# Kernel optimization log

Measured on AMD Instinct MI355X. Metric: run time of the kernel, lower is better.

## Reference

```python
import jax, jax.numpy as jnp
import numpy as np

N = 50000      # num nodes
E = 1_200_000  # num edges
NID = 92       # node_input_dim
ED = 1         # edge_input_dim
H = 64         # hidden_dim
L = 5          # num_layers
EMB = 64       # embedding_dim
G = 256        # num graphs in batch
EPS = 1e-5


def _glorot(key, shape):
    fan_in, fan_out = shape[-2], shape[-1]
    lim = float(np.sqrt(6.0 / (fan_in + fan_out)))
    return jax.random.uniform(key, shape, jnp.float32, -lim, lim)


def setup_inputs() -> dict:
    key = jax.random.key(0)
    ks = jax.random.split(key, 16)
    inp = {
        "x": jax.random.normal(ks[0], (N, NID), jnp.float32),
        "edge_attr": jax.random.uniform(ks[1], (E, ED), jnp.float32),
        "edge_index": jax.random.randint(ks[2], (2, E), 0, N, jnp.int32),
        "batch": jnp.sort(jax.random.randint(ks[3], (N,), 0, G, jnp.int32)),
        # node embedding
        "node_W": _glorot(ks[4], (NID, H)),
        "node_b": jnp.zeros((H,), jnp.float32),
        # per-layer message net: Linear(2H+ED,H) -> BN -> SiLU -> Linear(H,H)
        "msg_W1": _glorot(ks[5], (L, 2 * H + ED, H)),
        "msg_b1": jnp.zeros((L, H), jnp.float32),
        "msg_g1": jnp.ones((L, H), jnp.float32),
        "msg_be1": jnp.zeros((L, H), jnp.float32),
        "msg_W2": _glorot(ks[6], (L, H, H)),
        "msg_b2": jnp.zeros((L, H), jnp.float32),
        # per-layer update net: Linear(2H,H) -> BN -> SiLU
        "upd_W": _glorot(ks[7], (L, 2 * H, H)),
        "upd_b": jnp.zeros((L, H), jnp.float32),
        "upd_g": jnp.ones((L, H), jnp.float32),
        "upd_be": jnp.zeros((L, H), jnp.float32),
        # output projection
        "out_W": _glorot(ks[8], (H, EMB)),
        "out_b": jnp.zeros((EMB,), jnp.float32),
    }
    return inp


def _bn(z, g, b):
    # BatchNorm1d, training-mode batch statistics (biased variance), eps=1e-5
    mu = jnp.mean(z, axis=0)
    var = jnp.var(z, axis=0)
    return (z - mu) * jax.lax.rsqrt(var + EPS) * g + b


def reference(x, edge_attr, node_W, node_b, msg_W1, msg_b1, msg_g1, msg_be1,
              msg_W2, msg_b2, upd_W, upd_b, upd_g, upd_be, out_W, out_b,
              edge_index, batch):
    src, dst = edge_index[0], edge_index[1]  # PyG: x_j = x[src], x_i = x[dst]
    h = x @ node_W + node_b                  # [N, H]
    deg = jax.ops.segment_sum(jnp.ones((E,), h.dtype), dst, num_segments=N)
    deg = jnp.maximum(deg, 1.0)[:, None]     # mean aggregation denominator
    for l in range(L):
        # message: cat([x_i, x_j, edge_attr]) -> Linear -> BN -> SiLU -> Linear
        m = jnp.concatenate([h[dst], h[src], edge_attr], axis=1)  # [E, 2H+ED]
        m = _bn(m @ msg_W1[l] + msg_b1[l], msg_g1[l], msg_be1[l])
        m = jax.nn.silu(m) @ msg_W2[l] + msg_b2[l]                # [E, H]
        # aggregate: scatter-mean to destination nodes
        agg = jax.ops.segment_sum(m, dst, num_segments=N) / deg   # [N, H]
        # update: cat([x, agg]) -> Linear -> BN -> SiLU
        u = jnp.concatenate([h, agg], axis=1) @ upd_W[l] + upd_b[l]
        h = jax.nn.silu(_bn(u, upd_g[l], upd_be[l]))              # [N, H]
    # global mean pool over graphs
    cnt = jnp.maximum(jax.ops.segment_sum(jnp.ones((N,), h.dtype), batch, num_segments=G), 1.0)
    g = jax.ops.segment_sum(h, batch, num_segments=G) / cnt[:, None]  # [G, H]
    return jax.nn.silu(g @ out_W + out_b)                              # [G, EMB]
```

## Files before the change

kernel.cpp:

```cpp
#include <hip/hip_runtime.h>
#include <hip/hip_bf16.h>

#define NN 50000
#define EE 1200000
#define GG 256
#define LL 5

__device__ __forceinline__ float silu_f(float x) {
    return x * __builtin_amdgcn_rcpf(1.0f + __expf(-x));
}
__device__ __forceinline__ int rfl(int x) { return __builtin_amdgcn_readfirstlane(x); }

__global__ __launch_bounds__(256) void k_hist(const int* __restrict__ ei, int* __restrict__ fill, int E) {
    int e = blockIdx.x * 256 + threadIdx.x;
    if (e < E) atomicAdd(&fill[ei[E + e]], 1);
}

__global__ __launch_bounds__(256) void k_scan_blk(int* __restrict__ fill, int* __restrict__ rowptr,
                                                  float* __restrict__ degf, int* __restrict__ bsum, int n) {
    __shared__ int wsum[4];
    int tid = threadIdx.x, lane = tid & 63, wid = tid >> 6;
    int i = blockIdx.x * 256 + tid;
    int v = (i < n) ? fill[i] : 0;
    int x = v;
    #pragma unroll
    for (int off = 1; off < 64; off <<= 1) {
        int t = __shfl_up(x, off);
        if (lane >= off) x += t;
    }
    if (lane == 63) wsum[wid] = x;
    __syncthreads();
    int waveoff = 0;
    if (wid > 0) waveoff += wsum[0];
    if (wid > 1) waveoff += wsum[1];
    if (wid > 2) waveoff += wsum[2];
    int inc = x + waveoff;
    if (i < n) {
        rowptr[i + 1] = inc;
        degf[i] = (float)(v > 0 ? v : 1);
        fill[i] = 0;
    }
    if (tid == 255) bsum[blockIdx.x] = inc;
}

__global__ __launch_bounds__(256) void k_scan_top(int* __restrict__ bsum, int B) {
    __shared__ int wsum[4];
    int tid = threadIdx.x, lane = tid & 63, wid = tid >> 6;
    int v = (tid < B) ? bsum[tid] : 0;
    int x = v;
    #pragma unroll
    for (int off = 1; off < 64; off <<= 1) {
        int t = __shfl_up(x, off);
        if (lane >= off) x += t;
    }
    if (lane == 63) wsum[wid] = x;
    __syncthreads();
    int waveoff = 0;
    if (wid > 0) waveoff += wsum[0];
    if (wid > 1) waveoff += wsum[1];
    if (wid > 2) waveoff += wsum[2];
    if (tid < B) bsum[tid] = x + waveoff;
}

__global__ __launch_bounds__(256) void k_scan_add(const int* __restrict__ bsum, int* __restrict__ rowptr, int n) {
    int b = blockIdx.x;
    int i = b * 256 + threadIdx.x;
    if (i < n) {
        int add = (b > 0) ? bsum[b - 1] : 0;
        rowptr[i + 1] += add;
    }
    if (i == 0) rowptr[0] = 0;
}

__global__ __launch_bounds__(256) void k_scatter(const int* __restrict__ ei, const float* __restrict__ ea,
                                                 const int* __restrict__ rowptr, int* __restrict__ fill,
                                                 unsigned int* __restrict__ edata, int E) {
    int e = blockIdx.x * 256 + threadIdx.x;
    if (e < E) {
        int d = ei[E + e];
        int pos = atomicAdd(&fill[d], 1);
        int idx = rowptr[d] + pos;
        int ea15 = (int)(ea[e] * 32768.0f + 0.5f);
        if (ea15 > 32767) ea15 = 32767;
        edata[idx] = ((unsigned int)ea15 << 17) | (unsigned int)ei[e];
    }
}

__global__ __launch_bounds__(256) void k_fold(const float* __restrict__ msg_W2, const float* __restrict__ msg_b2,
                                              const float* __restrict__ upd_W, float* __restrict__ W2p,
                                              float* __restrict__ b2p) {
    int l = blockIdx.x;
    const float* W2 = msg_W2 + (size_t)l * 4096;
    const float* U2 = upd_W + (size_t)l * 8192 + 4096;
    int lane = threadIdx.x & 63, wid = threadIdx.x >> 6;
    for (int ii = 0; ii < 16; ii++) {
        int i = rfl(wid * 16 + ii);
        float acc = 0.0f;
        for (int k = 0; k < 64; k++) acc = fmaf(W2[i * 64 + k], U2[k * 64 + lane], acc);
        W2p[(size_t)l * 4096 + i * 64 + lane] = acc;
    }
    if (wid == 0) {
        float acc = 0.0f;
        for (int k = 0; k < 64; k++) acc = fmaf(msg_b2[l * 64 + k], U2[k * 64 + lane], acc);
        b2p[l * 64 + lane] = acc;
    }
}

__global__ __launch_bounds__(256) void k_node_emb(const float* __restrict__ x, const float* __restrict__ W,
                                                  const float* __restrict__ b, float* __restrict__ h, int n) {
    __shared__ float sW[92 * 64];
    for (int i = threadIdx.x; i < 92 * 64; i += 256) sW[i] = W[i];
    __syncthreads();
    int lane = threadIdx.x & 63;
    int gw = (blockIdx.x * 256 + threadIdx.x) >> 6;
    int nw = (gridDim.x * 256) >> 6;
    float bj = b[lane];
    int tiles = n >> 3;
    for (int t = gw; t < tiles; t += nw) {
        int rb = rfl(t << 3);
        float acc[8];
        #pragma unroll
        for (int r = 0; r < 8; r++) acc[r] = bj;
        for (int kb = 0; kb < 80; kb += 16) {
            float wv[16];
            #pragma unroll
            for (int t2 = 0; t2 < 16; t2++) wv[t2] = sW[(kb + t2) * 64 + lane];
            #pragma unroll
            for (int r = 0; r < 8; r++) {
                const float* xr = x + (size_t)(rb + r) * 92 + kb;
                #pragma unroll
                for (int t2 = 0; t2 < 16; t2++) acc[r] = fmaf(xr[t2], wv[t2], acc[r]);
            }
        }
        {
            float wv[12];
            #pragma unroll
            for (int t2 = 0; t2 < 12; t2++) wv[t2] = sW[(80 + t2) * 64 + lane];
            #pragma unroll
            for (int r = 0; r < 8; r++) {
                const float* xr = x + (size_t)(rb + r) * 92 + 80;
                #pragma unroll
                for (int t2 = 0; t2 < 12; t2++) acc[r] = fmaf(xr[t2], wv[t2], acc[r]);
            }
        }
        #pragma unroll
        for (int r = 0; r < 8; r++) h[(size_t)(rb + r) * 64 + lane] = acc[r];
    }
}

__global__ __launch_bounds__(256) void k_node_pre(const float* __restrict__ h, const float* __restrict__ W1,
                                                  const float* __restrict__ b1, float* __restrict__ Hd,
                                                  _Float16* __restrict__ Hs, int n) {
    __shared__ float sA[4096], sB[4096];
    for (int i = threadIdx.x; i < 4096; i += 256) { sA[i] = W1[i]; sB[i] = W1[4096 + i]; }
    __syncthreads();
    int lane = threadIdx.x & 63;
    int gw = (blockIdx.x * 256 + threadIdx.x) >> 6;
    int nw = (gridDim.x * 256) >> 6;
    float bj = b1[lane];
    int tiles = n >> 3;
    for (int t = gw; t < tiles; t += nw) {
        int rb = rfl(t << 3);
        float accA[8], accB[8];
        #pragma unroll
        for (int r = 0; r < 8; r++) { accA[r] = bj; accB[r] = 0.0f; }
        for (int kb = 0; kb < 64; kb += 16) {
            float wA[16], wB[16];
            #pragma unroll
            for (int t2 = 0; t2 < 16; t2++) { wA[t2] = sA[(kb + t2) * 64 + lane]; wB[t2] = sB[(kb + t2) * 64 + lane]; }
            #pragma unroll
            for (int r = 0; r < 8; r++) {
                const float* hr = h + (size_t)(rb + r) * 64 + kb;
                #pragma unroll
                for (int t2 = 0; t2 < 16; t2++) {
                    float hk = hr[t2];
                    accA[r] = fmaf(hk, wA[t2], accA[r]);
                    accB[r] = fmaf(hk, wB[t2], accB[r]);
                }
            }
        }
        #pragma unroll
        for (int r = 0; r < 8; r++) {
            Hd[(size_t)(rb + r) * 64 + lane] = accA[r];
            Hs[(size_t)(rb + r) * 64 + lane] = (_Float16)accB[r];
        }
    }
}

__global__ __launch_bounds__(256) void k_bn_pre(const float* __restrict__ u, const float* __restrict__ usum,
                                                const float* __restrict__ usq, const float* __restrict__ g,
                                                const float* __restrict__ be, const float* __restrict__ W1,
                                                const float* __restrict__ b1, float* __restrict__ h,
                                                float* __restrict__ Hd, _Float16* __restrict__ Hs,
                                                int n, float invN) {
    __shared__ float sA[4096], sB[4096];
    __shared__ float sH[4][8][64];
    for (int i = threadIdx.x; i < 4096; i += 256) { sA[i] = W1[i]; sB[i] = W1[4096 + i]; }
    __syncthreads();
    int lane = threadIdx.x & 63, wid = threadIdx.x >> 6;
    float mean = usum[lane] * invN;
    float var = usq[lane] * invN - mean * mean;
    float inv = rsqrtf(var + 1e-5f);
    float sc = inv * g[lane];
    float sh = fmaf(-mean, sc, be[lane]);
    float bj = b1[lane];
    int gw = (blockIdx.x * 256 + threadIdx.x) >> 6;
    int nw = (gridDim.x * 256) >> 6;
    int tiles = n >> 3;
    for (int t = gw; t < tiles; t += nw) {
        int rb = rfl(t << 3);
        #pragma unroll
        for (int r = 0; r < 8; r++) {
            float uv = u[(size_t)(rb + r) * 64 + lane];
            float hv = silu_f(fmaf(uv, sc, sh));
            h[(size_t)(rb + r) * 64 + lane] = hv;
            sH[wid][r][lane] = hv;
        }
        float accA[8], accB[8];
        #pragma unroll
        for (int r = 0; r < 8; r++) { accA[r] = bj; accB[r] = 0.0f; }
        for (int k = 0; k < 64; k += 2) {
            float wA0 = sA[k * 64 + lane],       wB0 = sB[k * 64 + lane];
            float wA1 = sA[(k + 1) * 64 + lane], wB1 = sB[(k + 1) * 64 + lane];
            #pragma unroll
            for (int r = 0; r < 8; r++) {
                float h0 = sH[wid][r][k], h1 = sH[wid][r][k + 1];
                accA[r] = fmaf(h0, wA0, accA[r]);
                accB[r] = fmaf(h0, wB0, accB[r]);
                accA[r] = fmaf(h1, wA1, accA[r]);
                accB[r] = fmaf(h1, wB1, accB[r]);
            }
        }
        #pragma unroll
        for (int r = 0; r < 8; r++) {
            Hd[(size_t)(rb + r) * 64 + lane] = accA[r];
            Hs[(size_t)(rb + r) * 64 + lane] = (_Float16)accB[r];
        }
    }
}

__global__ __launch_bounds__(256) void k_edge_stats(const float* __restrict__ Hd, const _Float16* __restrict__ Hs,
                                                    const int* __restrict__ rowptr, const unsigned int* __restrict__ edata,
                                                    const float* __restrict__ w1e,
                                                    float* __restrict__ esum, float* __restrict__ esq, int n) {
    __shared__ float rs[4][64], rq[4][64];
    int wid = threadIdx.x >> 6, lane = threadIdx.x & 63;
    int gw = (blockIdx.x * 256 + threadIdx.x) >> 6;
    int nw = (gridDim.x * 256) >> 6;
    float wj = w1e[lane] * (1.0f / 32768.0f);
    float s = 0.0f, q = 0.0f;
    for (int node = gw; node < n; node += nw) {
        int nu = rfl(node);
        int e0 = rowptr[nu], e1 = rowptr[nu + 1];
        if (e0 == e1) continue;
        float hd = Hd[(size_t)nu * 64 + lane];
        int e = e0;
        for (; e + 16 <= e1; e += 16) {
            float hs[16], av[16];
            #pragma unroll
            for (int j = 0; j < 16; j++) {
                unsigned int p = edata[e + j];
                int sidx = rfl((int)(p & 0x1FFFFu));
                av[j] = (float)rfl((int)(p >> 17));
                hs[j] = (float)Hs[(size_t)sidx * 64 + lane];
            }
            #pragma unroll
            for (int j = 0; j < 16; j++) {
                float z = fmaf(av[j], wj, hd) + hs[j];
                s += z;
                q = fmaf(z, z, q);
            }
        }
        for (; e + 8 <= e1; e += 8) {
            float hs[8], av[8];
            #pragma unroll
            for (int j = 0; j < 8; j++) {
                unsigned int p = edata[e + j];
                int sidx = rfl((int)(p & 0x1FFFFu));
                av[j] = (float)rfl((int)(p >> 17));
                hs[j] = (float)Hs[(size_t)sidx * 64 + lane];
            }
            #pragma unroll
            for (int j = 0; j < 8; j++) {
                float z = fmaf(av[j], wj, hd) + hs[j];
                s += z;
                q = fmaf(z, z, q);
            }
        }
        for (; e < e1; e++) {
            unsigned int p = edata[e];
            int sidx = rfl((int)(p & 0x1FFFFu));
            float a = (float)rfl((int)(p >> 17));
            float z = fmaf(a, wj, hd) + (float)Hs[(size_t)sidx * 64 + lane];
            s += z;
            q = fmaf(z, z, q);
        }
    }
    rs[wid][lane] = s; rq[wid][lane] = q;
    __syncthreads();
    if (wid == 0) {
        float ts = rs[0][lane] + rs[1][lane] + rs[2][lane] + rs[3][lane];
        float tq = rq[0][lane] + rq[1][lane] + rq[2][lane] + rq[3][lane];
        atomicAdd(&esum[lane], ts);
        atomicAdd(&esq[lane], tq);
    }
}

__global__ __launch_bounds__(256) void k_agg_upd(const float* __restrict__ Hd, const _Float16* __restrict__ Hs,
                                                 const int* __restrict__ rowptr, const unsigned int* __restrict__ edata,
                                                 const float* __restrict__ w1e,
                                                 const float* __restrict__ esum, const float* __restrict__ esq,
                                                 const float* __restrict__ g1, const float* __restrict__ be1,
                                                 const float* __restrict__ degf,
                                                 const float* __restrict__ h, const float* __restrict__ U1,
                                                 const float* __restrict__ W2p, const float* __restrict__ b2p,
                                                 const float* __restrict__ ub,
                                                 float* __restrict__ u, float* __restrict__ usum,
                                                 float* __restrict__ usq, int n, float invE) {
    __shared__ float sU[4096], sP[4096];
    __shared__ float2 sHA[4][4][64];
    for (int i = threadIdx.x; i < 4096; i += 256) { sU[i] = U1[i]; sP[i] = W2p[i]; }
    __syncthreads();
    int lane = threadIdx.x & 63, wid = threadIdx.x >> 6;
    float mean = esum[lane] * invE;
    float var = esq[lane] * invE - mean * mean;
    float inv = rsqrtf(var + 1e-5f);
    float sc = inv * g1[lane];
    float sh = fmaf(-mean, sc, be1[lane]);
    float wj = w1e[lane] * (1.0f / 32768.0f);
    float b2j = b2p[lane], ubj = ub[lane];
    int gw = (blockIdx.x * 256 + threadIdx.x) >> 6;
    int nw = (gridDim.x * 256) >> 6;
    float s = 0.0f, q = 0.0f;
    int tiles = n >> 2;
    for (int t = gw; t < tiles; t += nw) {
        int rb = rfl(t << 2);
        float gate[4];
        for (int r = 0; r < 4; r++) {
            int nu = rb + r;
            int e0 = rowptr[nu], e1 = rowptr[nu + 1];
            gate[r] = (e1 > e0) ? 1.0f : 0.0f;
            float hd = Hd[(size_t)nu * 64 + lane];
            float acc = 0.0f;
            int e = e0;
            for (; e + 16 <= e1; e += 16) {
                float hs[16], av[16];
                #pragma unroll
                for (int j = 0; j < 16; j++) {
                    unsigned int p = edata[e + j];
                    int sidx = rfl((int)(p & 0x1FFFFu));
                    av[j] = (float)rfl((int)(p >> 17));
                    hs[j] = (float)Hs[(size_t)sidx * 64 + lane];
                }
                #pragma unroll
                for (int j = 0; j < 16; j++) {
                    float z = fmaf(av[j], wj, hd) + hs[j];
                    acc += silu_f(fmaf(z, sc, sh));
                }
            }
            for (; e + 8 <= e1; e += 8) {
                float hs[8], av[8];
                #pragma unroll
                for (int j = 0; j < 8; j++) {
                    unsigned int p = edata[e + j];
                    int sidx = rfl((int)(p & 0x1FFFFu));
                    av[j] = (float)rfl((int)(p >> 17));
                    hs[j] = (float)Hs[(size_t)sidx * 64 + lane];
                }
                #pragma unroll
                for (int j = 0; j < 8; j++) {
                    float z = fmaf(av[j], wj, hd) + hs[j];
                    acc += silu_f(fmaf(z, sc, sh));
                }
            }
            for (; e < e1; e++) {
                unsigned int p = edata[e];
                int sidx = rfl((int)(p & 0x1FFFFu));
                float a = (float)rfl((int)(p >> 17));
                float z = fmaf(a, wj, hd) + (float)Hs[(size_t)sidx * 64 + lane];
                acc += silu_f(fmaf(z, sc, sh));
            }
            float hv = h[(size_t)nu * 64 + lane];
            sHA[wid][r][lane] = make_float2(hv, acc / degf[nu]);
        }
        float accu[4];
        #pragma unroll
        for (int r = 0; r < 4; r++) accu[r] = fmaf(gate[r], b2j, ubj);
        for (int k = 0; k < 64; k++) {
            float wU = sU[k * 64 + lane], wP = sP[k * 64 + lane];
            #pragma unroll
            for (int r = 0; r < 4; r++) {
                float2 ha = sHA[wid][r][k];
                accu[r] = fmaf(ha.x, wU, accu[r]);
                accu[r] = fmaf(ha.y, wP, accu[r]);
            }
        }
        #pragma unroll
        for (int r = 0; r < 4; r++) {
            u[(size_t)(rb + r) * 64 + lane] = accu[r];
            s += accu[r];
            q = fmaf(accu[r], accu[r], q);
        }
    }
    {
        float* my = (float*)&sHA[wid][0][0];
        my[lane] = s;
        my[64 + lane] = q;
    }
    __syncthreads();
    if (wid == 0) {
        float ts = 0.0f, tq = 0.0f;
        #pragma unroll
        for (int w = 0; w < 4; w++) {
            const float* b = (const float*)&sHA[w][0][0];
            ts += b[lane];
            tq += b[64 + lane];
        }
        atomicAdd(&usum[lane], ts);
        atomicAdd(&usq[lane], tq);
    }
}

__global__ __launch_bounds__(256) void k_bn_pool(const float* __restrict__ u, const float* __restrict__ usum,
                                                 const float* __restrict__ usq, const float* __restrict__ g,
                                                 const float* __restrict__ be, const int* __restrict__ batch,
                                                 float* __restrict__ gsum, float* __restrict__ gcnt,
                                                 int n, float invN) {
    __shared__ float ssc[64], ssh[64];
    if (threadIdx.x < 64) {
        int j = threadIdx.x;
        float mean = usum[j] * invN;
        float var = usq[j] * invN - mean * mean;
        float inv = rsqrtf(var + 1e-5f);
        float sc = inv * g[j];
        ssc[j] = sc;
        ssh[j] = fmaf(-mean, sc, be[j]);
    }
    __syncthreads();
    int lane = threadIdx.x & 63;
    int gw = (blockIdx.x * 256 + threadIdx.x) >> 6;
    int nw = (gridDim.x * 256) >> 6;
    int per = (n + nw - 1) / nw;
    int start = gw * per;
    int end = start + per; if (end > n) end = n;
    if (start >= end) return;
    float sc = ssc[lane], sh = ssh[lane];
    int cur = batch[start];
    float acc = 0.0f, c = 0.0f;
    for (int i = start; i < end; i++) {
        int b = batch[i];
        if (b != cur) {
            atomicAdd(&gsum[(size_t)cur * 64 + lane], acc);
            if (lane == 0) atomicAdd(&gcnt[cur], c);
            cur = b; acc = 0.0f; c = 0.0f;
        }
        float y = fmaf(u[(size_t)i * 64 + lane], sc, sh);
        acc += silu_f(y);
        c += 1.0f;
    }
    atomicAdd(&gsum[(size_t)cur * 64 + lane], acc);
    if (lane == 0) atomicAdd(&gcnt[cur], c);
}

__global__ __launch_bounds__(256) void k_out(const float* __restrict__ gsum, const float* __restrict__ gcnt,
                                             const float* __restrict__ OW, const float* __restrict__ ob,
                                             float* __restrict__ out, int G) {
    __shared__ float sW[4096];
    for (int i = threadIdx.x; i < 4096; i += 256) sW[i] = OW[i];
    __syncthreads();
    int lane = threadIdx.x & 63;
    int gw = (blockIdx.x * 256 + threadIdx.x) >> 6;
    int nw = (gridDim.x * 256) >> 6;
    for (int g = gw; g < G; g += nw) {
        int gu = rfl(g);
        float c = gcnt[gu]; if (c < 1.0f) c = 1.0f;
        float ci = 1.0f / c;
        float acc = ob[lane];
        const float* gr = gsum + (size_t)gu * 64;
        #pragma unroll
        for (int k = 0; k < 64; k++) acc = fmaf(gr[k] * ci, sW[k * 64 + lane], acc);
        out[(size_t)gu * 64 + lane] = silu_f(acc);
    }
}

extern "C" void kernel_launch(void* const* d_in, const int* in_sizes, int n_in,
                              void* d_out, int out_size, void* d_ws, size_t ws_size,
                              hipStream_t stream) {
    const int N = NN, E = EE, G = GG, L = LL;
    const float* x         = (const float*)d_in[0];
    const float* edge_attr = (const float*)d_in[1];
    const int*   edge_index= (const int*)d_in[2];
    const int*   batch     = (const int*)d_in[3];
    const float* node_W    = (const float*)d_in[4];
    const float* node_b    = (const float*)d_in[5];
    const float* msg_W1    = (const float*)d_in[6];
    const float* msg_b1    = (const float*)d_in[7];
    const float* msg_g1    = (const float*)d_in[8];
    const float* msg_be1   = (const float*)d_in[9];
    const float* msg_W2    = (const float*)d_in[10];
    const float* msg_b2    = (const float*)d_in[11];
    const float* upd_W     = (const float*)d_in[12];
    const float* upd_b     = (const float*)d_in[13];
    const float* upd_g     = (const float*)d_in[14];
    const float* upd_be    = (const float*)d_in[15];
    const float* out_W     = (const float*)d_in[16];
    const float* out_b     = (const float*)d_in[17];
    float* out = (float*)d_out;

    char* ws = (char*)d_ws;
    size_t off = 0;
    auto alloc = [&](size_t b) { size_t o = off; off = (off + b + 255) & ~(size_t)255; return o; };
    float* h    = (float*)(ws + alloc((size_t)N * 64 * 4));
    float* Hd   = (float*)(ws + alloc((size_t)N * 64 * 4));
    _Float16* Hs = (_Float16*)(ws + alloc((size_t)N * 64 * 2));
    unsigned int* edata = (unsigned int*)(ws + alloc((size_t)E * 4));
    int* rowptr = (int*)  (ws + alloc((size_t)(N + 1) * 4));
    float* degf = (float*)(ws + alloc((size_t)N * 4));
    float* W2p  = (float*)(ws + alloc((size_t)L * 4096 * 4));
    float* b2p  = (float*)(ws + alloc((size_t)L * 64 * 4));
    int* bsum   = (int*)  (ws + alloc((size_t)256 * 4));
    size_t zero_begin = off;
    int*   fill = (int*)  (ws + alloc((size_t)N * 4));
    float* stats= (float*)(ws + alloc((size_t)L * 4 * 64 * 4));
    float* gsum = (float*)(ws + alloc((size_t)(G * 64 + G) * 4));
    size_t zero_end = off;
    float* gcnt = gsum + (size_t)G * 64;
    float* u = Hd;

    hipMemsetAsync(ws + zero_begin, 0, zero_end - zero_begin, stream);

    const int SB = (N + 255) / 256;
    k_hist<<<(E + 255) / 256, 256, 0, stream>>>(edge_index, fill, E);
    k_scan_blk<<<SB, 256, 0, stream>>>(fill, rowptr, degf, bsum, N);
    k_scan_top<<<1, 256, 0, stream>>>(bsum, SB);
    k_scan_add<<<SB, 256, 0, stream>>>(bsum, rowptr, N);
    k_scatter<<<(E + 255) / 256, 256, 0, stream>>>(edge_index, edge_attr, rowptr, fill, edata, E);

    k_fold<<<L, 256, 0, stream>>>(msg_W2, msg_b2, upd_W, W2p, b2p);
    k_node_emb<<<1024, 256, 0, stream>>>(x, node_W, node_b, h, N);

    k_node_pre<<<1024, 256, 0, stream>>>(h, msg_W1, msg_b1, Hd, Hs, N);

    for (int l = 0; l < L; l++) {
        const float* W1  = msg_W1 + (size_t)l * 129 * 64;
        const float* w1e = W1 + 128 * 64;
        float* esum = stats + (size_t)l * 256;
        float* esq  = esum + 64;
        float* usum = esum + 128;
        float* usq  = esum + 192;
        k_edge_stats<<<2048, 256, 0, stream>>>(Hd, Hs, rowptr, edata, w1e, esum, esq, N);
        k_agg_upd<<<1024, 256, 0, stream>>>(Hd, Hs, rowptr, edata, w1e, esum, esq,
                                            msg_g1 + l * 64, msg_be1 + l * 64, degf,
                                            h, upd_W + (size_t)l * 8192, W2p + (size_t)l * 4096,
                                            b2p + (size_t)l * 64, upd_b + l * 64,
                                            u, usum, usq, N, 1.0f / E);
        if (l < L - 1) {
            const float* W1n = msg_W1 + (size_t)(l + 1) * 129 * 64;
            k_bn_pre<<<1024, 256, 0, stream>>>(u, usum, usq, upd_g + l * 64, upd_be + l * 64,
                                               W1n, msg_b1 + (l + 1) * 64, h, Hd, Hs, N, 1.0f / N);
        } else {
            k_bn_pool<<<256, 256, 0, stream>>>(u, usum, usq, upd_g + l * 64, upd_be + l * 64,
                                               batch, gsum, gcnt, N, 1.0f / N);
        }
    }

    k_out<<<64, 256, 0, stream>>>(gsum, gcnt, out_W, out_b, out, G);
}
```

Baseline: 1.187 ms.

## Precompute update-net h·U1 term in node pre-pass and stage x rows in LDS

The h-part of the update linear (h @ U1 + ub) moves out of the edge aggregation kernel and into the node pre-pass kernels, which now compute three 64x64 products per node and write a new Hu buffer. The aggregation kernel then only multiplies the aggregated messages by the folded W2' matrix, which shrinks its LDS footprint and inner loop, and its grid grows. The node embedding kernel stages each wave's 8 input rows in shared memory with float4 loads instead of scalar global reads. The pre-pass kernels use 4-row tiles with more LDS and an extra N×64 float buffer that must be written and read, and h is still written in full.

```diff
diff --git a/kernel.cpp b/kernel.cpp
--- a/kernel.cpp
+++ b/kernel.cpp
@@ -109,15 +109,21 @@
 __global__ __launch_bounds__(256) void k_node_emb(const float* __restrict__ x, const float* __restrict__ W,
                                                   const float* __restrict__ b, float* __restrict__ h, int n) {
     __shared__ float sW[92 * 64];
+    __shared__ float sX[4][736];
     for (int i = threadIdx.x; i < 92 * 64; i += 256) sW[i] = W[i];
     __syncthreads();
-    int lane = threadIdx.x & 63;
+    int lane = threadIdx.x & 63, wid = threadIdx.x >> 6;
     int gw = (blockIdx.x * 256 + threadIdx.x) >> 6;
     int nw = (gridDim.x * 256) >> 6;
     float bj = b[lane];
     int tiles = n >> 3;
     for (int t = gw; t < tiles; t += nw) {
         int rb = rfl(t << 3);
+        const float4* xb = (const float4*)(x + (size_t)rb * 92);
+        float4* sx4 = (float4*)&sX[wid][0];
+        sx4[lane] = xb[lane];
+        sx4[lane + 64] = xb[lane + 64];
+        if (lane < 56) sx4[lane + 128] = xb[lane + 128];
         float acc[8];
         #pragma unroll
         for (int r = 0; r < 8; r++) acc[r] = bj;
@@ -127,9 +133,8 @@
             for (int t2 = 0; t2 < 16; t2++) wv[t2] = sW[(kb + t2) * 64 + lane];
             #pragma unroll
             for (int r = 0; r < 8; r++) {
-                const float* xr = x + (size_t)(rb + r) * 92 + kb;
-                #pragma unroll
-                for (int t2 = 0; t2 < 16; t2++) acc[r] = fmaf(xr[t2], wv[t2], acc[r]);
+                #pragma unroll
+                for (int t2 = 0; t2 < 16; t2++) acc[r] = fmaf(sX[wid][r * 92 + kb + t2], wv[t2], acc[r]);
             }
         }
         {
@@ -138,9 +143,8 @@
             for (int t2 = 0; t2 < 12; t2++) wv[t2] = sW[(80 + t2) * 64 + lane];
             #pragma unroll
             for (int r = 0; r < 8; r++) {
-                const float* xr = x + (size_t)(rb + r) * 92 + 80;
-                #pragma unroll
-                for (int t2 = 0; t2 < 12; t2++) acc[r] = fmaf(xr[t2], wv[t2], acc[r]);
+                #pragma unroll
+                for (int t2 = 0; t2 < 12; t2++) acc[r] = fmaf(sX[wid][r * 92 + 80 + t2], wv[t2], acc[r]);
             }
         }
         #pragma unroll
@@ -149,40 +153,48 @@
 }
 
 __global__ __launch_bounds__(256) void k_node_pre(const float* __restrict__ h, const float* __restrict__ W1,
-                                                  const float* __restrict__ b1, float* __restrict__ Hd,
-                                                  _Float16* __restrict__ Hs, int n) {
-    __shared__ float sA[4096], sB[4096];
-    for (int i = threadIdx.x; i < 4096; i += 256) { sA[i] = W1[i]; sB[i] = W1[4096 + i]; }
-    __syncthreads();
-    int lane = threadIdx.x & 63;
-    int gw = (blockIdx.x * 256 + threadIdx.x) >> 6;
-    int nw = (gridDim.x * 256) >> 6;
-    float bj = b1[lane];
-    int tiles = n >> 3;
+                                                  const float* __restrict__ b1, const float* __restrict__ U1,
+                                                  const float* __restrict__ ub, float* __restrict__ Hd,
+                                                  _Float16* __restrict__ Hs, float* __restrict__ Hu, int n) {
+    __shared__ float sA[4096], sB[4096], sU[4096];
+    __shared__ float sH[4][256];
+    for (int i = threadIdx.x; i < 4096; i += 256) { sA[i] = W1[i]; sB[i] = W1[4096 + i]; sU[i] = U1[i]; }
+    __syncthreads();
+    int lane = threadIdx.x & 63, wid = threadIdx.x >> 6;
+    int gw = (blockIdx.x * 256 + threadIdx.x) >> 6;
+    int nw = (gridDim.x * 256) >> 6;
+    float bj = b1[lane], uj = ub[lane];
+    int tiles = n >> 2;
     for (int t = gw; t < tiles; t += nw) {
-        int rb = rfl(t << 3);
-        float accA[8], accB[8];
-        #pragma unroll
-        for (int r = 0; r < 8; r++) { accA[r] = bj; accB[r] = 0.0f; }
-        for (int kb = 0; kb < 64; kb += 16) {
-            float wA[16], wB[16];
-            #pragma unroll
-            for (int t2 = 0; t2 < 16; t2++) { wA[t2] = sA[(kb + t2) * 64 + lane]; wB[t2] = sB[(kb + t2) * 64 + lane]; }
-            #pragma unroll
-            for (int r = 0; r < 8; r++) {
-                const float* hr = h + (size_t)(rb + r) * 64 + kb;
-                #pragma unroll
-                for (int t2 = 0; t2 < 16; t2++) {
-                    float hk = hr[t2];
+        int rb = rfl(t << 2);
+        ((float4*)&sH[wid][0])[lane] = ((const float4*)(h + (size_t)rb * 64))[lane];
+        float accA[4], accB[4], accU[4];
+        #pragma unroll
+        for (int r = 0; r < 4; r++) { accA[r] = bj; accB[r] = 0.0f; accU[r] = uj; }
+        for (int kb = 0; kb < 64; kb += 8) {
+            float wA[8], wB[8], wU[8];
+            #pragma unroll
+            for (int t2 = 0; t2 < 8; t2++) {
+                wA[t2] = sA[(kb + t2) * 64 + lane];
+                wB[t2] = sB[(kb + t2) * 64 + lane];
+                wU[t2] = sU[(kb + t2) * 64 + lane];
+            }
+            #pragma unroll
+            for (int r = 0; r < 4; r++) {
+                #pragma unroll
+                for (int t2 = 0; t2 < 8; t2++) {
+                    float hk = sH[wid][r * 64 + kb + t2];
                     accA[r] = fmaf(hk, wA[t2], accA[r]);
                     accB[r] = fmaf(hk, wB[t2], accB[r]);
+                    accU[r] = fmaf(hk, wU[t2], accU[r]);
                 }
             }
         }
         #pragma unroll
-        for (int r = 0; r < 8; r++) {
+        for (int r = 0; r < 4; r++) {
             Hd[(size_t)(rb + r) * 64 + lane] = accA[r];
             Hs[(size_t)(rb + r) * 64 + lane] = (_Float16)accB[r];
+            Hu[(size_t)(rb + r) * 64 + lane] = accU[r];
         }
     }
 }
@@ -190,12 +202,13 @@
 __global__ __launch_bounds__(256) void k_bn_pre(const float* __restrict__ u, const float* __restrict__ usum,
                                                 const float* __restrict__ usq, const float* __restrict__ g,
                                                 const float* __restrict__ be, const float* __restrict__ W1,
-                                                const float* __restrict__ b1, float* __restrict__ h,
+                                                const float* __restrict__ b1, const float* __restrict__ U1,
+                                                const float* __restrict__ ub, float* __restrict__ h,
                                                 float* __restrict__ Hd, _Float16* __restrict__ Hs,
-                                                int n, float invN) {
-    __shared__ float sA[4096], sB[4096];
-    __shared__ float sH[4][8][64];
-    for (int i = threadIdx.x; i < 4096; i += 256) { sA[i] = W1[i]; sB[i] = W1[4096 + i]; }
+                                                float* __restrict__ Hu, int n, float invN) {
+    __shared__ float sA[4096], sB[4096], sU[4096];
+    __shared__ float sH[4][256];
+    for (int i = threadIdx.x; i < 4096; i += 256) { sA[i] = W1[i]; sB[i] = W1[4096 + i]; sU[i] = U1[i]; }
     __syncthreads();
     int lane = threadIdx.x & 63, wid = threadIdx.x >> 6;
     float mean = usum[lane] * invN;
@@ -203,38 +216,46 @@
     float inv = rsqrtf(var + 1e-5f);
     float sc = inv * g[lane];
     float sh = fmaf(-mean, sc, be[lane]);
-    float bj = b1[lane];
-    int gw = (blockIdx.x * 256 + threadIdx.x) >> 6;
-    int nw = (gridDim.x * 256) >> 6;
-    int tiles = n >> 3;
+    float bj = b1[lane], uj = ub[lane];
+    int gw = (blockIdx.x * 256 + threadIdx.x) >> 6;
+    int nw = (gridDim.x * 256) >> 6;
+    int tiles = n >> 2;
     for (int t = gw; t < tiles; t += nw) {
-        int rb = rfl(t << 3);
-        #pragma unroll
-        for (int r = 0; r < 8; r++) {
+        int rb = rfl(t << 2);
+        #pragma unroll
+        for (int r = 0; r < 4; r++) {
             float uv = u[(size_t)(rb + r) * 64 + lane];
             float hv = silu_f(fmaf(uv, sc, sh));
             h[(size_t)(rb + r) * 64 + lane] = hv;
-            sH[wid][r][lane] = hv;
-        }
-        float accA[8], accB[8];
-        #pragma unroll
-        for (int r = 0; r < 8; r++) { accA[r] = bj; accB[r] = 0.0f; }
-        for (int k = 0; k < 64; k += 2) {
-            float wA0 = sA[k * 64 + lane],       wB0 = sB[k * 64 + lane];
-            float wA1 = sA[(k + 1) * 64 + lane], wB1 = sB[(k + 1) * 64 + lane];
-            #pragma unroll
-            for (int r = 0; r < 8; r++) {
-                float h0 = sH[wid][r][k], h1 = sH[wid][r][k + 1];
-                accA[r] = fmaf(h0, wA0, accA[r]);
-                accB[r] = fmaf(h0, wB0, accB[r]);
-                accA[r] = fmaf(h1, wA1, accA[r]);
-                accB[r] = fmaf(h1, wB1, accB[r]);
-            }
-        }
-        #pragma unroll
-        for (int r = 0; r < 8; r++) {
+            sH[wid][r * 64 + lane] = hv;
+        }
+        float accA[4], accB[4], accU[4];
+        #pragma unroll
+        for (int r = 0; r < 4; r++) { accA[r] = bj; accB[r] = 0.0f; accU[r] = uj; }
+        for (int kb = 0; kb < 64; kb += 8) {
+            float wA[8], wB[8], wU[8];
+            #pragma unroll
+            for (int t2 = 0; t2 < 8; t2++) {
+                wA[t2] = sA[(kb + t2) * 64 + lane];
+                wB[t2] = sB[(kb + t2) * 64 + lane];
+                wU[t2] = sU[(kb + t2) * 64 + lane];
+            }
+            #pragma unroll
+            for (int r = 0; r < 4; r++) {
+                #pragma unroll
+                for (int t2 = 0; t2 < 8; t2++) {
+                    float hk = sH[wid][r * 64 + kb + t2];
+                    accA[r] = fmaf(hk, wA[t2], accA[r]);
+                    accB[r] = fmaf(hk, wB[t2], accB[r]);
+                    accU[r] = fmaf(hk, wU[t2], accU[r]);
+                }
+            }
+        }
+        #pragma unroll
+        for (int r = 0; r < 4; r++) {
             Hd[(size_t)(rb + r) * 64 + lane] = accA[r];
             Hs[(size_t)(rb + r) * 64 + lane] = (_Float16)accB[r];
+            Hu[(size_t)(rb + r) * 64 + lane] = accU[r];
         }
     }
 }
@@ -312,14 +333,13 @@
                                                  const float* __restrict__ esum, const float* __restrict__ esq,
                                                  const float* __restrict__ g1, const float* __restrict__ be1,
                                                  const float* __restrict__ degf,
-                                                 const float* __restrict__ h, const float* __restrict__ U1,
-                                                 const float* __restrict__ W2p, const float* __restrict__ b2p,
-                                                 const float* __restrict__ ub,
+                                                 const float* __restrict__ Hu, const float* __restrict__ W2p,
+                                                 const float* __restrict__ b2p,
                                                  float* __restrict__ u, float* __restrict__ usum,
                                                  float* __restrict__ usq, int n, float invE) {
-    __shared__ float sU[4096], sP[4096];
-    __shared__ float2 sHA[4][4][64];
-    for (int i = threadIdx.x; i < 4096; i += 256) { sU[i] = U1[i]; sP[i] = W2p[i]; }
+    __shared__ float sP[4096];
+    __shared__ float sAgg[4][4][64];
+    for (int i = threadIdx.x; i < 4096; i += 256) sP[i] = W2p[i];
     __syncthreads();
     int lane = threadIdx.x & 63, wid = threadIdx.x >> 6;
     float mean = esum[lane] * invE;
@@ -328,18 +348,17 @@
     float sc = inv * g1[lane];
     float sh = fmaf(-mean, sc, be1[lane]);
     float wj = w1e[lane] * (1.0f / 32768.0f);
-    float b2j = b2p[lane], ubj = ub[lane];
+    float b2j = b2p[lane];
     int gw = (blockIdx.x * 256 + threadIdx.x) >> 6;
     int nw = (gridDim.x * 256) >> 6;
     float s = 0.0f, q = 0.0f;
     int tiles = n >> 2;
     for (int t = gw; t < tiles; t += nw) {
         int rb = rfl(t << 2);
-        float gate[4];
+        float base[4];
         for (int r = 0; r < 4; r++) {
             int nu = rb + r;
             int e0 = rowptr[nu], e1 = rowptr[nu + 1];
-            gate[r] = (e1 > e0) ? 1.0f : 0.0f;
             float hd = Hd[(size_t)nu * 64 + lane];
             float acc = 0.0f;
             int e = e0;
@@ -380,20 +399,16 @@
                 float z = fmaf(a, wj, hd) + (float)Hs[(size_t)sidx * 64 + lane];
                 acc += silu_f(fmaf(z, sc, sh));
             }
-            float hv = h[(size_t)nu * 64 + lane];
-            sHA[wid][r][lane] = make_float2(hv, acc / degf[nu]);
+            sAgg[wid][r][lane] = acc / degf[nu];
+            base[r] = Hu[(size_t)nu * 64 + lane] + ((e1 > e0) ? b2j : 0.0f);
         }
         float accu[4];
         #pragma unroll
-        for (int r = 0; r < 4; r++) accu[r] = fmaf(gate[r], b2j, ubj);
+        for (int r = 0; r < 4; r++) accu[r] = base[r];
         for (int k = 0; k < 64; k++) {
-            float wU = sU[k * 64 + lane], wP = sP[k * 64 + lane];
-            #pragma unroll
-            for (int r = 0; r < 4; r++) {
-                float2 ha = sHA[wid][r][k];
-                accu[r] = fmaf(ha.x, wU, accu[r]);
-                accu[r] = fmaf(ha.y, wP, accu[r]);
-            }
+            float wP = sP[k * 64 + lane];
+            #pragma unroll
+            for (int r = 0; r < 4; r++) accu[r] = fmaf(sAgg[wid][r][k], wP, accu[r]);
         }
         #pragma unroll
         for (int r = 0; r < 4; r++) {
@@ -403,7 +418,7 @@
         }
     }
     {
-        float* my = (float*)&sHA[wid][0][0];
+        float* my = &sAgg[wid][0][0];
         my[lane] = s;
         my[64 + lane] = q;
     }
@@ -412,7 +427,7 @@
         float ts = 0.0f, tq = 0.0f;
         #pragma unroll
         for (int w = 0; w < 4; w++) {
-            const float* b = (const float*)&sHA[w][0][0];
+            const float* b = &sAgg[w][0][0];
             ts += b[lane];
             tq += b[64 + lane];
         }
@@ -513,6 +528,7 @@
     float* h    = (float*)(ws + alloc((size_t)N * 64 * 4));
     float* Hd   = (float*)(ws + alloc((size_t)N * 64 * 4));
     _Float16* Hs = (_Float16*)(ws + alloc((size_t)N * 64 * 2));
+    float* Hu   = (float*)(ws + alloc((size_t)N * 64 * 4));
     unsigned int* edata = (unsigned int*)(ws + alloc((size_t)E * 4));
     int* rowptr = (int*)  (ws + alloc((size_t)(N + 1) * 4));
     float* degf = (float*)(ws + alloc((size_t)N * 4));
@@ -539,7 +555,7 @@
     k_fold<<<L, 256, 0, stream>>>(msg_W2, msg_b2, upd_W, W2p, b2p);
     k_node_emb<<<1024, 256, 0, stream>>>(x, node_W, node_b, h, N);
 
-    k_node_pre<<<1024, 256, 0, stream>>>(h, msg_W1, msg_b1, Hd, Hs, N);
+    k_node_pre<<<768, 256, 0, stream>>>(h, msg_W1, msg_b1, upd_W, upd_b, Hd, Hs, Hu, N);
 
     for (int l = 0; l < L; l++) {
         const float* W1  = msg_W1 + (size_t)l * 129 * 64;
@@ -549,15 +565,16 @@
         float* usum = esum + 128;
         float* usq  = esum + 192;
         k_edge_stats<<<2048, 256, 0, stream>>>(Hd, Hs, rowptr, edata, w1e, esum, esq, N);
-        k_agg_upd<<<1024, 256, 0, stream>>>(Hd, Hs, rowptr, edata, w1e, esum, esq,
+        k_agg_upd<<<1536, 256, 0, stream>>>(Hd, Hs, rowptr, edata, w1e, esum, esq,
                                             msg_g1 + l * 64, msg_be1 + l * 64, degf,
-                                            h, upd_W + (size_t)l * 8192, W2p + (size_t)l * 4096,
-                                            b2p + (size_t)l * 64, upd_b + l * 64,
+                                            Hu, W2p + (size_t)l * 4096, b2p + (size_t)l * 64,
                                             u, usum, usq, N, 1.0f / E);
         if (l < L - 1) {
             const float* W1n = msg_W1 + (size_t)(l + 1) * 129 * 64;
-            k_bn_pre<<<1024, 256, 0, stream>>>(u, usum, usq, upd_g + l * 64, upd_be + l * 64,
-                                               W1n, msg_b1 + (l + 1) * 64, h, Hd, Hs, N, 1.0f / N);
+            k_bn_pre<<<768, 256, 0, stream>>>(u, usum, usq, upd_g + l * 64, upd_be + l * 64,
+                                              W1n, msg_b1 + (l + 1) * 64,
+                                              upd_W + (size_t)(l + 1) * 8192, upd_b + (l + 1) * 64,
+                                              h, Hd, Hs, Hu, N, 1.0f / N);
         } else {
             k_bn_pool<<<256, 256, 0, stream>>>(u, usum, usq, upd_g + l * 64, upd_be + l * 64,
                                                batch, gsum, gcnt, N, 1.0f / N);
```

Result: slower. 1.387 ms (+16.9%).
